# Performance work log

Measured on AMD Instinct MI355X. Metric: run time of the kernel, lower is better.

The kernel has to match this reference:

```python
import jax, jax.numpy as jnp
import numpy as np

LAMBDA = 0.5
ALPHA_PRE = 1.0
ALPHA_DA = 1.0

B, N, C, T, O = 8, 1024, 64, 12, 64


def setup_inputs() -> dict:
    key = jax.random.key(0)
    ks = jax.random.split(key, 10)
    s = 0.1  # keep tanh out of deep saturation, like xavier-init scales
    return {
        "x": jax.random.normal(ks[0], (B, N, C, T), dtype=jnp.float32),
        "static_adj": jax.random.uniform(ks[1], (N, N), dtype=jnp.float32) / N,
        "W0": jax.random.normal(ks[2], (C, O), dtype=jnp.float32) * s,
        "b0": jax.random.normal(ks[3], (O,), dtype=jnp.float32) * s,
        "Ws": jax.random.normal(ks[4], (T, C, O), dtype=jnp.float32) * s,
        "bs": jax.random.normal(ks[5], (T, O), dtype=jnp.float32) * s,
        "Wd": jax.random.normal(ks[6], (T, C, O), dtype=jnp.float32) * s,
        "bd": jax.random.normal(ks[7], (T, O), dtype=jnp.float32) * s,
        "E1": jax.random.normal(ks[8], (T, N, O), dtype=jnp.float32) * s,
        "E2": jax.random.normal(ks[9], (T, N, O), dtype=jnp.float32) * s,
    }


def reference(x, static_adj, W0, b0, Ws, bs, Wd, bd, E1, E2):
    # x: [B,N,C,T] -> [T,B,N,C] so the per-timestep layers vectorize over leading T.
    xt = jnp.transpose(x, (3, 0, 1, 2))  # [T,B,N,C]
    n = xt.shape[2]

    # shared top-level linear
    x0 = jnp.einsum('tbnc,co->tbno', xt, W0) + b0  # [T,B,N,O]

    # static GCN per timestep: linear(static_adj @ x_t)
    sagg = jnp.einsum('nm,tbmc->tbnc', static_adj, xt)
    static_out = jnp.einsum('tbnc,tco->tbno', sagg, Ws) + bs[:, None, None, :]

    # dynamic GCN: base = linear_t(x_t)
    base = jnp.einsum('tbnc,tco->tbno', xt, Wd) + bd[:, None, None, :]
    DE1 = jnp.tanh(ALPHA_PRE * (base * E1[:, None]))  # [T,B,N,O]
    DE2 = jnp.tanh(ALPHA_PRE * (base * E2[:, None]))
    # cross = DE1@DE2^T - DE2@DE1^T = M - M^T
    M = jnp.einsum('tbno,tbmo->tbnm', DE1, DE2)  # [T,B,N,N]
    DA = jax.nn.relu(jnp.tanh(ALPHA_DA * (M - jnp.swapaxes(M, -1, -2))))

    # symmetric degree normalization of (DA + I)
    DA = DA + jnp.eye(n, dtype=DA.dtype)
    rowsum = jnp.clip(DA.sum(axis=-1), 1e-12, None)
    d_inv_sqrt = rowsum ** -0.5
    DA = DA * d_inv_sqrt[..., :, None] * d_inv_sqrt[..., None, :]

    dagg = jnp.einsum('tbnm,tbmc->tbnc', DA, xt)
    dyn_out = jnp.einsum('tbnc,tco->tbno', dagg, Wd) + bd[:, None, None, :]

    fused = (LAMBDA - 0.025) * static_out + (1.0 - LAMBDA - 0.025) * dyn_out + 0.05 * x0
    return jnp.transpose(fused, (1, 2, 3, 0))  # [B,N,O,T]
```

## Files before the change

### kernel.cpp

```cpp
#include <hip/hip_runtime.h>

#define BB 8
#define NN 1024
#define CC 64
#define TT 12
#define OO 64

typedef unsigned short u16;
typedef __attribute__((ext_vector_type(8))) short s16x8;
typedef __attribute__((ext_vector_type(4))) float f32x4;
typedef __attribute__((ext_vector_type(4))) unsigned int u32x4;

__device__ __forceinline__ u16 f2bu(float f){
  union { float f; unsigned u; } v; v.f = f;
  unsigned r = v.u + 0x7FFFu + ((v.u >> 16) & 1u);
  return (u16)(r >> 16);
}
__device__ __forceinline__ float b2f(u16 h){
  union { unsigned u; float f; } v; v.u = ((unsigned)h) << 16; return v.f;
}
__device__ __forceinline__ float relu_tanh(float d){
  float e = __expf(2.0f * d);
  return fmaxf(1.0f - 2.0f * __builtin_amdgcn_rcpf(e + 1.0f), 0.0f);
}
__device__ __forceinline__ float tanh_sgn(float x){
  float ax = fabsf(x);
  float e = __expf(2.0f * ax);
  float t = 1.0f - 2.0f * __builtin_amdgcn_rcpf(e + 1.0f);
  return x < 0.0f ? -t : t;
}

#define MFMA16(a,b,c) __builtin_amdgcn_mfma_f32_16x16x32_bf16((a),(b),(c),0,0,0)

__device__ __forceinline__ s16x8 ld72(const u16* s, int row0, int ko, int lane){
  return *(const s16x8*)(s + (row0 + (lane & 15)) * 72 + ko + ((lane >> 4) << 3));
}

__global__ __launch_bounds__(256) void k0_transpose(const float* __restrict__ x,
                                                    u16* __restrict__ xt){
  const int n = blockIdx.x, b = blockIdx.y;
  __shared__ float s[CC*TT];
  const float* src = x + (size_t)(b*NN + n)*CC*TT;
  for (int k = threadIdx.x; k < CC*TT; k += 256) s[k] = src[k];
  __syncthreads();
  for (int k = threadIdx.x; k < CC*TT; k += 256){
    const int t = k >> 6, c = k & 63;
    xt[(((size_t)t*BB + b)*NN + n)*CC + c] = f2bu(s[c*TT + t]);
  }
}

__global__ __launch_bounds__(256) void kadj(const float* __restrict__ adj,
                                            u16* __restrict__ adjb){
  const size_t i = ((size_t)blockIdx.x*256 + threadIdx.x)*4;
  const float4 v = *(const float4*)(adj + i);
  u16 o0=f2bu(v.x), o1=f2bu(v.y), o2=f2bu(v.z), o3=f2bu(v.w);
  adjb[i]=o0; adjb[i+1]=o1; adjb[i+2]=o2; adjb[i+3]=o3;
}

__global__ __launch_bounds__(256) void k1_de(const u16* __restrict__ xt,
    const float* __restrict__ Wd, const float* __restrict__ bd,
    const float* __restrict__ E1, const float* __restrict__ E2,
    u16* __restrict__ DE1g, u16* __restrict__ DE2g){
  __shared__ __align__(16) u16 sWd[64*72];
  const int tid = threadIdx.x, lane = tid & 63, wid = tid >> 6;
  const int l15 = lane & 15, lr4 = lane >> 4;
  const int it = blockIdx.x, b = blockIdx.y, t = blockIdx.z;
  const int n0 = it * 64;
  for (int k = tid; k < 4096; k += 256){
    const int o = k & 63, c = k >> 6;
    sWd[o*72 + c] = f2bu(Wd[(size_t)t*4096 + c*64 + o]);
  }
  __syncthreads();
  const size_t tb = (size_t)t*BB + b;
  const u16* gx = xt + (tb*NN + n0)*CC;
  const int wrow = wid * 16;
  const f32x4 fz = {0.f,0.f,0.f,0.f};
  f32x4 acc[4] = {fz, fz, fz, fz};
  #pragma unroll
  for (int ks = 0; ks < 2; ++ks){
    const int ko = ks*32;
    const s16x8 a = *(const s16x8*)(gx + (wrow + l15)*CC + ko + (lr4 << 3));
    #pragma unroll
    for (int v = 0; v < 4; ++v)
      acc[v] = MFMA16(a, ld72(sWd, v*16, ko, lane), acc[v]);
  }
  #pragma unroll
  for (int v = 0; v < 4; ++v){
    const int o = v*16 + l15;
    const float bdv = bd[t*OO + o];
    #pragma unroll
    for (int e = 0; e < 4; ++e){
      const int n = n0 + wrow + (lr4 << 2) + e;
      const float base = acc[v][e] + bdv;
      const size_t eo = ((size_t)t*NN + n)*OO + o;
      const size_t so = (tb*NN + n)*OO + o;
      DE1g[so] = f2bu(tanh_sgn(base * E1[eo]));
      DE2g[so] = f2bu(tanh_sgn(base * E2[eo]));
    }
  }
}

__global__ __launch_bounds__(256) void k2a(const u16* __restrict__ DE1g,
    const u16* __restrict__ DE2g, float* __restrict__ dinv){
  __shared__ __align__(16) u16 sB1[64*72], sB2[64*72];
  const int tid = threadIdx.x, lane = tid & 63, wid = tid >> 6;
  const int l15 = lane & 15, lr4 = lane >> 4;
  const int nwg = 16*BB*TT;
  const int logical = ((int)blockIdx.x & 7)*(nwg >> 3) + ((int)blockIdx.x >> 3);
  const int ti = logical & 15;
  const size_t tb = (size_t)(logical >> 4);
  const u16* g1 = DE1g + tb*NN*OO;
  const u16* g2 = DE2g + tb*NN*OO;
  const int i0 = ti * 64;
  for (int k = tid; k < 512; k += 256){
    const int r = k >> 3, c = (k & 7) << 3;
    *(s16x8*)(sB1 + r*72 + c) = *(const s16x8*)(g1 + (size_t)(i0 + r)*OO + c);
    s16x8 v = *(const s16x8*)(g2 + (size_t)(i0 + r)*OO + c);
    u32x4 w = *(u32x4*)&v; w ^= 0x80008000u;
    *(u32x4*)(sB2 + r*72 + c) = w;
  }
  __syncthreads();
  const int wrow = wid * 16;
  s16x8 a1[2], na2[2];
  #pragma unroll
  for (int ks = 0; ks < 2; ++ks){
    a1[ks]  = ld72(sB1, wrow, ks*32, lane);
    na2[ks] = ld72(sB2, wrow, ks*32, lane);
  }
  const int srow = tid >> 2, sc0 = (tid & 3) << 4;
  s16x8 pB1a,pB1b, pB2a,pB2b;
#define LOADT(TJ) do { \
    pB1a = *(const s16x8*)(g2 + (size_t)((TJ)*64 + srow)*OO + sc0); \
    pB1b = *(const s16x8*)(g2 + (size_t)((TJ)*64 + srow)*OO + sc0 + 8); \
    pB2a = *(const s16x8*)(g1 + (size_t)((TJ)*64 + srow)*OO + sc0); \
    pB2b = *(const s16x8*)(g1 + (size_t)((TJ)*64 + srow)*OO + sc0 + 8); \
  } while (0)
  LOADT(0);
  float rp[4] = {0.f,0.f,0.f,0.f};
  const f32x4 fz = {0.f,0.f,0.f,0.f};
  __syncthreads();
  for (int tj = 0; tj < 16; ++tj){
    *(s16x8*)(sB1 + srow*72 + sc0)     = pB1a;
    *(s16x8*)(sB1 + srow*72 + sc0 + 8) = pB1b;
    *(s16x8*)(sB2 + srow*72 + sc0)     = pB2a;
    *(s16x8*)(sB2 + srow*72 + sc0 + 8) = pB2b;
    __syncthreads();
    if (tj < 15) LOADT(tj + 1);
    f32x4 z[4];
    #pragma unroll
    for (int v = 0; v < 4; ++v){
      z[v] = MFMA16(a1[0],  ld72(sB1, v*16, 0,  lane), fz);
      z[v] = MFMA16(na2[0], ld72(sB2, v*16, 0,  lane), z[v]);
      z[v] = MFMA16(a1[1],  ld72(sB1, v*16, 32, lane), z[v]);
      z[v] = MFMA16(na2[1], ld72(sB2, v*16, 32, lane), z[v]);
    }
    #pragma unroll
    for (int v = 0; v < 4; ++v)
      #pragma unroll
      for (int e = 0; e < 4; ++e)
        rp[e] += relu_tanh(z[v][e]);
    __syncthreads();
  }
#undef LOADT
  #pragma unroll
  for (int e = 0; e < 4; ++e){
    float r = rp[e];
    r += __shfl_xor(r, 1); r += __shfl_xor(r, 2);
    r += __shfl_xor(r, 4); r += __shfl_xor(r, 8);
    if (l15 == 0)
      dinv[tb*NN + i0 + wrow + (lr4 << 2) + e] = rsqrtf(r + 1.0f);
  }
}

__global__ __launch_bounds__(256) void k3b(const u16* __restrict__ xt,
    const float* __restrict__ Wd, const float* __restrict__ Ws,
    const float* __restrict__ W0, const float* __restrict__ bd,
    const float* __restrict__ bs, const float* __restrict__ b0,
    const float* __restrict__ dinv, u16* __restrict__ xdvT,
    u16* __restrict__ xswT, u16* __restrict__ x0w){
  __shared__ __align__(16) u16 sW[64*72];
  const int tid = threadIdx.x, lane = tid & 63, wid = tid >> 6;
  const int l15 = lane & 15, lr4 = lane >> 4;
  const int it = blockIdx.x, b = blockIdx.y, t = blockIdx.z;
  const size_t tb = (size_t)t*BB + b;
  const int n0 = it * 128, wrow = wid * 32;
  const float* dvb = dinv + tb*NN + n0;
  float dis[2][4];
  #pragma unroll
  for (int u = 0; u < 2; ++u)
    #pragma unroll
    for (int e = 0; e < 4; ++e)
      dis[u][e] = dvb[wrow + u*16 + (lr4 << 2) + e];
  float badd[4];
  #pragma unroll
  for (int v = 0; v < 4; ++v){
    const int o = v*16 + l15;
    badd[v] = 0.475f*(bd[t*OO + o] + bs[t*OO + o]) + 0.05f*b0[o];
  }
  const u16* gx = xt + (tb*NN + n0)*CC;
  const f32x4 fz = {0.f,0.f,0.f,0.f};
  for (int pass = 0; pass < 3; ++pass){
    __syncthreads();
    {
      const float* Wsrc = (pass == 0) ? (Wd + (size_t)t*4096)
                        : (pass == 1) ? (Ws + (size_t)t*4096) : W0;
      const float scale = (pass == 2) ? 0.05f : 0.475f;
      for (int k = tid; k < 4096; k += 256){
        const int o = k & 63, c = k >> 6;
        sW[o*72 + c] = f2bu(scale * Wsrc[c*64 + o]);
      }
    }
    __syncthreads();
    f32x4 acc[2][4];
    #pragma unroll
    for (int u = 0; u < 2; ++u)
      #pragma unroll
      for (int v = 0; v < 4; ++v) acc[u][v] = fz;
    #pragma unroll
    for (int ks = 0; ks < 2; ++ks){
      const int ko = ks*32;
      s16x8 bw[4];
      #pragma unroll
      for (int v = 0; v < 4; ++v) bw[v] = ld72(sW, v*16, ko, lane);
      #pragma unroll
      for (int u = 0; u < 2; ++u){
        const s16x8 a = *(const s16x8*)(gx + (wrow + u*16 + l15)*CC + ko + (lr4 << 3));
        #pragma unroll
        for (int v = 0; v < 4; ++v) acc[u][v] = MFMA16(a, bw[v], acc[u][v]);
      }
    }
    #pragma unroll
    for (int u = 0; u < 2; ++u)
      #pragma unroll
      for (int v = 0; v < 4; ++v){
        const int o = v*16 + l15;
        #pragma unroll
        for (int e = 0; e < 4; ++e){
          const int nl = wrow + u*16 + (lr4 << 2) + e;
          float val = acc[u][v][e];
          if (pass == 0)      xdvT[(tb*OO + o)*NN + n0 + nl] = f2bu(val * dis[u][e]);
          else if (pass == 1) xswT[(tb*OO + o)*NN + n0 + nl] = f2bu(val);
          else                x0w[(tb*NN + n0 + nl)*OO + o]  = f2bu(val + badd[v]);
        }
      }
  }
}

__global__ __launch_bounds__(256) void k4s(const u16* __restrict__ adjb,
    const u16* __restrict__ xswT, u16* __restrict__ outSta){
  __shared__ __align__(16) u16 sJ[64*72], sS[64*72];
  const int tid = threadIdx.x, lane = tid & 63, wid = tid >> 6;
  const int l15 = lane & 15, lr4 = lane >> 4;
  const int nwg = 16*BB*TT;
  const int logical = ((int)blockIdx.x & 7)*(nwg >> 3) + ((int)blockIdx.x >> 3);
  const int ti = logical / (BB*TT);
  const size_t tb = (size_t)(logical % (BB*TT));
  const u16* xs = xswT + tb*OO*NN;
  const int i0 = ti * 64, wrow = wid * 16;
  const int srow = tid >> 2, sc0 = (tid & 3) << 4;
  s16x8 pJa, pJb, pSa, pSb;
#define LOADS(TJ) do { \
    pJa = *(const s16x8*)(adjb + (size_t)(i0 + srow)*NN + (TJ)*64 + sc0); \
    pJb = *(const s16x8*)(adjb + (size_t)(i0 + srow)*NN + (TJ)*64 + sc0 + 8); \
    pSa = *(const s16x8*)(xs   + (size_t)srow*NN + (TJ)*64 + sc0); \
    pSb = *(const s16x8*)(xs   + (size_t)srow*NN + (TJ)*64 + sc0 + 8); \
  } while (0)
  LOADS(0);
  const f32x4 fz = {0.f,0.f,0.f,0.f};
  f32x4 as_[4] = {fz,fz,fz,fz};
  for (int tj = 0; tj < 16; ++tj){
    *(s16x8*)(sJ + srow*72 + sc0)     = pJa;
    *(s16x8*)(sJ + srow*72 + sc0 + 8) = pJb;
    *(s16x8*)(sS + srow*72 + sc0)     = pSa;
    *(s16x8*)(sS + srow*72 + sc0 + 8) = pSb;
    __syncthreads();
    if (tj < 15) LOADS(tj + 1);
    const s16x8 aJ0 = ld72(sJ, wrow, 0,  lane);
    const s16x8 aJ1 = ld72(sJ, wrow, 32, lane);
    #pragma unroll
    for (int v = 0; v < 4; ++v){
      as_[v] = MFMA16(aJ0, ld72(sS, v*16, 0,  lane), as_[v]);
      as_[v] = MFMA16(aJ1, ld72(sS, v*16, 32, lane), as_[v]);
    }
    __syncthreads();
  }
#undef LOADS
  #pragma unroll
  for (int v = 0; v < 4; ++v){
    const int o = v*16 + l15;
    #pragma unroll
    for (int e = 0; e < 4; ++e){
      const int n = i0 + wrow + (lr4 << 2) + e;
      outSta[(tb*NN + n)*OO + o] = f2bu(as_[v][e]);
    }
  }
}

__global__ __launch_bounds__(256) void k2bf(const u16* __restrict__ DE1g,
    const u16* __restrict__ DE2g, const u16* __restrict__ xdvT,
    const float* __restrict__ dinv, float* __restrict__ outT){
  __shared__ __align__(16) u16 sB1[64*72], sB2[64*72], sXD[64*72];
  __shared__ __align__(16) u16 bounce[4][16*72];
  const int tid = threadIdx.x, lane = tid & 63, wid = tid >> 6;
  const int l15 = lane & 15, lr4 = lane >> 4;
  const int nwg = 16*BB*TT;
  const int logical = ((int)blockIdx.x & 7)*(nwg >> 3) + ((int)blockIdx.x >> 3);
  const int ti = logical & 15;
  const size_t tb = (size_t)(logical >> 4);
  const u16* g1 = DE1g + tb*NN*OO;
  const u16* g2 = DE2g + tb*NN*OO;
  const u16* xd = xdvT + tb*OO*NN;
  const float* dv = dinv + tb*NN;
  const int i0 = ti * 64;
  for (int k = tid; k < 512; k += 256){
    const int r = k >> 3, c = (k & 7) << 3;
    *(s16x8*)(sB1 + r*72 + c) = *(const s16x8*)(g1 + (size_t)(i0 + r)*OO + c);
    s16x8 v = *(const s16x8*)(g2 + (size_t)(i0 + r)*OO + c);
    u32x4 w = *(u32x4*)&v; w ^= 0x80008000u;
    *(u32x4*)(sB2 + r*72 + c) = w;
  }
  __syncthreads();
  const int wrow = wid * 16;
  s16x8 a1[2], na2[2];
  #pragma unroll
  for (int ks = 0; ks < 2; ++ks){
    a1[ks]  = ld72(sB1, wrow, ks*32, lane);
    na2[ks] = ld72(sB2, wrow, ks*32, lane);
  }
  const int srow = tid >> 2, sc0 = (tid & 3) << 4;
  s16x8 pB1a,pB1b, pB2a,pB2b, pXDa,pXDb;
#define LOADT(TJ) do { \
    pB1a = *(const s16x8*)(g2 + (size_t)((TJ)*64 + srow)*OO + sc0); \
    pB1b = *(const s16x8*)(g2 + (size_t)((TJ)*64 + srow)*OO + sc0 + 8); \
    pB2a = *(const s16x8*)(g1 + (size_t)((TJ)*64 + srow)*OO + sc0); \
    pB2b = *(const s16x8*)(g1 + (size_t)((TJ)*64 + srow)*OO + sc0 + 8); \
    pXDa = *(const s16x8*)(xd + (size_t)srow*NN + (TJ)*64 + sc0); \
    pXDb = *(const s16x8*)(xd + (size_t)srow*NN + (TJ)*64 + sc0 + 8); \
  } while (0)
  LOADT(0);
  u16* wb = bounce[wid];
  const f32x4 fz = {0.f,0.f,0.f,0.f};
  f32x4 ad[4] = {fz,fz,fz,fz};
  __syncthreads();
  for (int tj = 0; tj < 16; ++tj){
    *(s16x8*)(sB1 + srow*72 + sc0)     = pB1a;
    *(s16x8*)(sB1 + srow*72 + sc0 + 8) = pB1b;
    *(s16x8*)(sB2 + srow*72 + sc0)     = pB2a;
    *(s16x8*)(sB2 + srow*72 + sc0 + 8) = pB2b;
    *(s16x8*)(sXD + srow*72 + sc0)     = pXDa;
    *(s16x8*)(sXD + srow*72 + sc0 + 8) = pXDb;
    __syncthreads();
    if (tj < 15) LOADT(tj + 1);
    f32x4 z[4];
    #pragma unroll
    for (int v = 0; v < 4; ++v){
      z[v] = MFMA16(a1[0],  ld72(sB1, v*16, 0,  lane), fz);
      z[v] = MFMA16(na2[0], ld72(sB2, v*16, 0,  lane), z[v]);
      z[v] = MFMA16(a1[1],  ld72(sB1, v*16, 32, lane), z[v]);
      z[v] = MFMA16(na2[1], ld72(sB2, v*16, 32, lane), z[v]);
    }
    #pragma unroll
    for (int v = 0; v < 4; ++v)
      #pragma unroll
      for (int e = 0; e < 4; ++e)
        wb[((lr4 << 2) + e)*72 + v*16 + l15] = f2bu(relu_tanh(z[v][e]));
    asm volatile("s_waitcnt lgkmcnt(0)" ::: "memory");
    __builtin_amdgcn_sched_barrier(0);
    s16x8 pa0 = ld72(wb, 0, 0,  lane);
    s16x8 pa1 = ld72(wb, 0, 32, lane);
    #pragma unroll
    for (int v = 0; v < 4; ++v){
      ad[v] = MFMA16(pa0, ld72(sXD, v*16, 0,  lane), ad[v]);
      ad[v] = MFMA16(pa1, ld72(sXD, v*16, 32, lane), ad[v]);
    }
    __syncthreads();
  }
#undef LOADT
  const int grow0 = i0 + wrow + (lr4 << 2);
  float disv[4];
  #pragma unroll
  for (int e = 0; e < 4; ++e) disv[e] = dv[grow0 + e];
  #pragma unroll
  for (int v = 0; v < 4; ++v){
    const int o = v*16 + l15;
    #pragma unroll
    for (int e = 0; e < 4; ++e){
      const float xw = b2f(xd[(size_t)o*NN + grow0 + e]);
      outT[(tb*NN + grow0 + e)*OO + o] = disv[e]*(ad[v][e] + xw);
    }
  }
}

__global__ __launch_bounds__(256) void k5(const float* __restrict__ outT,
                                          const u16* __restrict__ x0w,
                                          const u16* __restrict__ outSta,
                                          float* __restrict__ out){
  __shared__ float s[16*64*12];
  const int tid = threadIdx.x;
  const int nb = blockIdx.x, b = blockIdx.y;
  const int n0 = nb * 16;
  for (int t = 0; t < TT; ++t){
    for (int k = tid; k < 1024; k += 256){
      const int r = k >> 6, o = k & 63;
      const size_t idx = (((size_t)t*BB + b)*NN + n0 + r)*OO + o;
      s[(r*64 + o)*12 + t] = outT[idx] + b2f(x0w[idx]) + b2f(outSta[idx]);
    }
  }
  __syncthreads();
  float* dst = out + (size_t)(b*NN + n0)*OO*TT;
  for (int k = tid; k < 16*64*12; k += 256) dst[k] = s[k];
}

extern "C" void kernel_launch(void* const* d_in, const int* in_sizes, int n_in,
                              void* d_out, int out_size, void* d_ws, size_t ws_size,
                              hipStream_t stream) {
  const float* x   = (const float*)d_in[0];
  const float* adj = (const float*)d_in[1];
  const float* W0  = (const float*)d_in[2];
  const float* b0  = (const float*)d_in[3];
  const float* Ws  = (const float*)d_in[4];
  const float* bs  = (const float*)d_in[5];
  const float* Wd  = (const float*)d_in[6];
  const float* bd  = (const float*)d_in[7];
  const float* E1  = (const float*)d_in[8];
  const float* E2  = (const float*)d_in[9];
  float* out = (float*)d_out;

  char* w = (char*)d_ws;
  size_t off = 0;
  auto take = [&](size_t bytes) -> char* {
    char* p = w + off;
    off += bytes; off = (off + 255) & ~(size_t)255;
    return p;
  };
  const size_t NE = (size_t)TT*BB*NN*OO;
  u16*   xt    = (u16*)  take(NE*2);
  u16*   adjb  = (u16*)  take((size_t)NN*NN*2);
  u16*   DE1   = (u16*)  take(NE*2);
  u16*   DE2   = (u16*)  take(NE*2);
  float* dinv  = (float*)take((size_t)TT*BB*NN*4);
  u16*   xdvT  = (u16*)  take(NE*2);
  u16*   xswT  = (u16*)  take(NE*2);
  u16*   x0w   = (u16*)  take(NE*2);
  u16*   outSta= (u16*)  take(NE*2);
  float* outT  = (float*)take(NE*4);

  k0_transpose<<<dim3(NN, BB), 256, 0, stream>>>(x, xt);
  kadj<<<dim3((NN*NN)/1024), 256, 0, stream>>>(adj, adjb);
  k1_de<<<dim3(16, BB, TT), 256, 0, stream>>>(xt, Wd, bd, E1, E2, DE1, DE2);
  k2a<<<dim3(16*BB*TT), 256, 0, stream>>>(DE1, DE2, dinv);
  k3b<<<dim3(8, BB, TT), 256, 0, stream>>>(xt, Wd, Ws, W0, bd, bs, b0,
                                           dinv, xdvT, xswT, x0w);
  k4s<<<dim3(16*BB*TT), 256, 0, stream>>>(adjb, xswT, outSta);
  k2bf<<<dim3(16*BB*TT), 256, 0, stream>>>(DE1, DE2, xdvT, dinv, outT);
  k5<<<dim3(NN/16, BB), 256, 0, stream>>>(outT, x0w, outSta, out);
}
```

Baseline: 234.1 us.

## Exploit antisymmetry of cross matrix to halve degree computation in k2a

```diff
diff --git a/kernel.cpp b/kernel.cpp
--- a/kernel.cpp
+++ b/kernel.cpp
@@ -22,6 +22,10 @@
 __device__ __forceinline__ float relu_tanh(float d){
   float e = __expf(2.0f * d);
   return fmaxf(1.0f - 2.0f * __builtin_amdgcn_rcpf(e + 1.0f), 0.0f);
+}
+__device__ __forceinline__ float tanh_fast(float d){
+  float e = __expf(2.0f * d);
+  return 1.0f - 2.0f * __builtin_amdgcn_rcpf(e + 1.0f);
 }
 __device__ __forceinline__ float tanh_sgn(float x){
   float ax = fabsf(x);
@@ -55,6 +59,11 @@
   const float4 v = *(const float4*)(adj + i);
   u16 o0=f2bu(v.x), o1=f2bu(v.y), o2=f2bu(v.z), o3=f2bu(v.w);
   adjb[i]=o0; adjb[i+1]=o1; adjb[i+2]=o2; adjb[i+3]=o3;
+}
+
+__global__ __launch_bounds__(256) void kinit(float* __restrict__ rs){
+  const size_t i = (size_t)blockIdx.x*256 + threadIdx.x;
+  if (i < (size_t)TT*BB*NN) rs[i] = 1.0f;
 }
 
 __global__ __launch_bounds__(256) void k1_de(const u16* __restrict__ xt,
@@ -101,32 +110,41 @@
 }
 
 __global__ __launch_bounds__(256) void k2a(const u16* __restrict__ DE1g,
-    const u16* __restrict__ DE2g, float* __restrict__ dinv){
-  __shared__ __align__(16) u16 sB1[64*72], sB2[64*72];
+    const u16* __restrict__ DE2g, float* __restrict__ rowsum){
+  __shared__ __align__(16) u16 s1A[64*72], s2nA[64*72];
+  __shared__ __align__(16) u16 s1B[64*72], s2nB[64*72];
   const int tid = threadIdx.x, lane = tid & 63, wid = tid >> 6;
   const int l15 = lane & 15, lr4 = lane >> 4;
-  const int nwg = 16*BB*TT;
+  const int nwg = 8*BB*TT;
   const int logical = ((int)blockIdx.x & 7)*(nwg >> 3) + ((int)blockIdx.x >> 3);
-  const int ti = logical & 15;
-  const size_t tb = (size_t)(logical >> 4);
+  const int p = logical & 7;
+  const size_t tb = (size_t)(logical >> 3);
+  const int tiA = p, tiB = 15 - p;
   const u16* g1 = DE1g + tb*NN*OO;
   const u16* g2 = DE2g + tb*NN*OO;
-  const int i0 = ti * 64;
   for (int k = tid; k < 512; k += 256){
     const int r = k >> 3, c = (k & 7) << 3;
-    *(s16x8*)(sB1 + r*72 + c) = *(const s16x8*)(g1 + (size_t)(i0 + r)*OO + c);
-    s16x8 v = *(const s16x8*)(g2 + (size_t)(i0 + r)*OO + c);
-    u32x4 w = *(u32x4*)&v; w ^= 0x80008000u;
-    *(u32x4*)(sB2 + r*72 + c) = w;
+    *(s16x8*)(s1A + r*72 + c) = *(const s16x8*)(g1 + (size_t)(tiA*64 + r)*OO + c);
+    s16x8 vA = *(const s16x8*)(g2 + (size_t)(tiA*64 + r)*OO + c);
+    u32x4 wA = *(u32x4*)&vA; wA ^= 0x80008000u;
+    *(u32x4*)(s2nA + r*72 + c) = wA;
+    *(s16x8*)(s1B + r*72 + c) = *(const s16x8*)(g1 + (size_t)(tiB*64 + r)*OO + c);
+    s16x8 vB = *(const s16x8*)(g2 + (size_t)(tiB*64 + r)*OO + c);
+    u32x4 wB = *(u32x4*)&vB; wB ^= 0x80008000u;
+    *(u32x4*)(s2nB + r*72 + c) = wB;
   }
   __syncthreads();
   const int wrow = wid * 16;
-  s16x8 a1[2], na2[2];
+  s16x8 a1A[2], na2A[2], a1B[2], na2B[2];
   #pragma unroll
   for (int ks = 0; ks < 2; ++ks){
-    a1[ks]  = ld72(sB1, wrow, ks*32, lane);
-    na2[ks] = ld72(sB2, wrow, ks*32, lane);
-  }
+    a1A[ks]  = ld72(s1A,  wrow, ks*32, lane);
+    na2A[ks] = ld72(s2nA, wrow, ks*32, lane);
+    a1B[ks]  = ld72(s1B,  wrow, ks*32, lane);
+    na2B[ks] = ld72(s2nB, wrow, ks*32, lane);
+  }
+  u16* sJ1 = s1A;
+  u16* sJ2 = s2nA;
   const int srow = tid >> 2, sc0 = (tid & 3) << 4;
   s16x8 pB1a,pB1b, pB2a,pB2b;
 #define LOADT(TJ) do { \
@@ -135,40 +153,96 @@
     pB2a = *(const s16x8*)(g1 + (size_t)((TJ)*64 + srow)*OO + sc0); \
     pB2b = *(const s16x8*)(g1 + (size_t)((TJ)*64 + srow)*OO + sc0 + 8); \
   } while (0)
-  LOADT(0);
-  float rp[4] = {0.f,0.f,0.f,0.f};
+  LOADT(p);
+  float rpA[4] = {0.f,0.f,0.f,0.f}, rpB[4] = {0.f,0.f,0.f,0.f};
   const f32x4 fz = {0.f,0.f,0.f,0.f};
-  __syncthreads();
-  for (int tj = 0; tj < 16; ++tj){
-    *(s16x8*)(sB1 + srow*72 + sc0)     = pB1a;
-    *(s16x8*)(sB1 + srow*72 + sc0 + 8) = pB1b;
-    *(s16x8*)(sB2 + srow*72 + sc0)     = pB2a;
-    *(s16x8*)(sB2 + srow*72 + sc0 + 8) = pB2b;
+  float* rsg = rowsum + tb*NN;
+  __syncthreads();
+  for (int tj = p; tj < 16; ++tj){
+    *(s16x8*)(sJ1 + srow*72 + sc0)     = pB1a;
+    *(s16x8*)(sJ1 + srow*72 + sc0 + 8) = pB1b;
+    *(s16x8*)(sJ2 + srow*72 + sc0)     = pB2a;
+    *(s16x8*)(sJ2 + srow*72 + sc0 + 8) = pB2b;
     __syncthreads();
     if (tj < 15) LOADT(tj + 1);
-    f32x4 z[4];
+    s16x8 b1[4], b2[4], b1h[4], b2h[4];
     #pragma unroll
     for (int v = 0; v < 4; ++v){
-      z[v] = MFMA16(a1[0],  ld72(sB1, v*16, 0,  lane), fz);
-      z[v] = MFMA16(na2[0], ld72(sB2, v*16, 0,  lane), z[v]);
-      z[v] = MFMA16(a1[1],  ld72(sB1, v*16, 32, lane), z[v]);
-      z[v] = MFMA16(na2[1], ld72(sB2, v*16, 32, lane), z[v]);
-    }
-    #pragma unroll
-    for (int v = 0; v < 4; ++v)
-      #pragma unroll
-      for (int e = 0; e < 4; ++e)
-        rp[e] += relu_tanh(z[v][e]);
+      b1[v]  = ld72(sJ1, v*16, 0,  lane);
+      b2[v]  = ld72(sJ2, v*16, 0,  lane);
+      b1h[v] = ld72(sJ1, v*16, 32, lane);
+      b2h[v] = ld72(sJ2, v*16, 32, lane);
+    }
+    {
+      f32x4 z[4];
+      #pragma unroll
+      for (int v = 0; v < 4; ++v){
+        z[v] = MFMA16(a1A[0],  b1[v],  fz);
+        z[v] = MFMA16(na2A[0], b2[v],  z[v]);
+        z[v] = MFMA16(a1A[1],  b1h[v], z[v]);
+        z[v] = MFMA16(na2A[1], b2h[v], z[v]);
+      }
+      float colp[4] = {0.f,0.f,0.f,0.f};
+      #pragma unroll
+      for (int v = 0; v < 4; ++v)
+        #pragma unroll
+        for (int e = 0; e < 4; ++e){
+          const float th = tanh_fast(z[v][e]);
+          rpA[e]  += fmaxf(th, 0.f);
+          colp[v] += fmaxf(-th, 0.f);
+        }
+      if (tj > tiA){
+        #pragma unroll
+        for (int v = 0; v < 4; ++v){
+          float c = colp[v];
+          c += __shfl_xor(c, 16); c += __shfl_xor(c, 32);
+          if (lane < 16) atomicAdd(&rsg[tj*64 + v*16 + lane], c);
+        }
+      }
+    }
+    if (tj >= tiB){
+      f32x4 z[4];
+      #pragma unroll
+      for (int v = 0; v < 4; ++v){
+        z[v] = MFMA16(a1B[0],  b1[v],  fz);
+        z[v] = MFMA16(na2B[0], b2[v],  z[v]);
+        z[v] = MFMA16(a1B[1],  b1h[v], z[v]);
+        z[v] = MFMA16(na2B[1], b2h[v], z[v]);
+      }
+      float colp[4] = {0.f,0.f,0.f,0.f};
+      #pragma unroll
+      for (int v = 0; v < 4; ++v)
+        #pragma unroll
+        for (int e = 0; e < 4; ++e){
+          const float th = tanh_fast(z[v][e]);
+          rpB[e]  += fmaxf(th, 0.f);
+          colp[v] += fmaxf(-th, 0.f);
+        }
+      if (tj > tiB){
+        #pragma unroll
+        for (int v = 0; v < 4; ++v){
+          float c = colp[v];
+          c += __shfl_xor(c, 16); c += __shfl_xor(c, 32);
+          if (lane < 16) atomicAdd(&rsg[tj*64 + v*16 + lane], c);
+        }
+      }
+    }
     __syncthreads();
   }
 #undef LOADT
   #pragma unroll
   for (int e = 0; e < 4; ++e){
-    float r = rp[e];
+    float r = rpA[e];
     r += __shfl_xor(r, 1); r += __shfl_xor(r, 2);
     r += __shfl_xor(r, 4); r += __shfl_xor(r, 8);
-    if (l15 == 0)
-      dinv[tb*NN + i0 + wrow + (lr4 << 2) + e] = rsqrtf(r + 1.0f);
+    if (l15 == 0) atomicAdd(&rsg[tiA*64 + wrow + (lr4 << 2) + e], r);
+  }
+  #pragma unroll
+  for (int e = 0; e < 4; ++e){
+    float r = rpB[e];
+    r += __shfl_xor(r, 1); r += __shfl_xor(r, 2);
+    r += __shfl_xor(r, 4); r += __shfl_xor(r, 8);
+    if (l15 == 0) atomicAdd(&rsg[tiB*64 + wrow + (lr4 << 2) + e], r);
   }
 }
 
@@ -176,7 +250,7 @@
     const float* __restrict__ Wd, const float* __restrict__ Ws,
     const float* __restrict__ W0, const float* __restrict__ bd,
     const float* __restrict__ bs, const float* __restrict__ b0,
-    const float* __restrict__ dinv, u16* __restrict__ xdvT,
+    const float* __restrict__ rowsum, u16* __restrict__ xdvT,
     u16* __restrict__ xswT, u16* __restrict__ x0w){
   __shared__ __align__(16) u16 sW[64*72];
   const int tid = threadIdx.x, lane = tid & 63, wid = tid >> 6;
@@ -184,13 +258,13 @@
   const int it = blockIdx.x, b = blockIdx.y, t = blockIdx.z;
   const size_t tb = (size_t)t*BB + b;
   const int n0 = it * 128, wrow = wid * 32;
-  const float* dvb = dinv + tb*NN + n0;
+  const float* dvb = rowsum + tb*NN + n0;
   float dis[2][4];
   #pragma unroll
   for (int u = 0; u < 2; ++u)
     #pragma unroll
     for (int e = 0; e < 4; ++e)
-      dis[u][e] = dvb[wrow + u*16 + (lr4 << 2) + e];
+      dis[u][e] = rsqrtf(dvb[wrow + u*16 + (lr4 << 2) + e]);
   float badd[4];
   #pragma unroll
   for (int v = 0; v < 4; ++v){
@@ -298,7 +372,7 @@
 
 __global__ __launch_bounds__(256) void k2bf(const u16* __restrict__ DE1g,
     const u16* __restrict__ DE2g, const u16* __restrict__ xdvT,
-    const float* __restrict__ dinv, float* __restrict__ outT){
+    const float* __restrict__ rowsum, float* __restrict__ outT){
   __shared__ __align__(16) u16 sB1[64*72], sB2[64*72], sXD[64*72];
   __shared__ __align__(16) u16 bounce[4][16*72];
   const int tid = threadIdx.x, lane = tid & 63, wid = tid >> 6;
@@ -310,7 +384,7 @@
   const u16* g1 = DE1g + tb*NN*OO;
   const u16* g2 = DE2g + tb*NN*OO;
   const u16* xd = xdvT + tb*OO*NN;
-  const float* dv = dinv + tb*NN;
+  const float* dv = rowsum + tb*NN;
   const int i0 = ti * 64;
   for (int k = tid; k < 512; k += 256){
     const int r = k >> 3, c = (k & 7) << 3;
@@ -379,7 +453,7 @@
   const int grow0 = i0 + wrow + (lr4 << 2);
   float disv[4];
   #pragma unroll
-  for (int e = 0; e < 4; ++e) disv[e] = dv[grow0 + e];
+  for (int e = 0; e < 4; ++e) disv[e] = rsqrtf(dv[grow0 + e]);
   #pragma unroll
   for (int v = 0; v < 4; ++v){
     const int o = v*16 + l15;
@@ -438,7 +512,7 @@
   u16*   adjb  = (u16*)  take((size_t)NN*NN*2);
   u16*   DE1   = (u16*)  take(NE*2);
   u16*   DE2   = (u16*)  take(NE*2);
-  float* dinv  = (float*)take((size_t)TT*BB*NN*4);
+  float* rowsum= (float*)take((size_t)TT*BB*NN*4);
   u16*   xdvT  = (u16*)  take(NE*2);
   u16*   xswT  = (u16*)  take(NE*2);
   u16*   x0w   = (u16*)  take(NE*2);
@@ -447,11 +521,12 @@
 
   k0_transpose<<<dim3(NN, BB), 256, 0, stream>>>(x, xt);
   kadj<<<dim3((NN*NN)/1024), 256, 0, stream>>>(adj, adjb);
+  kinit<<<dim3((TT*BB*NN + 255)/256), 256, 0, stream>>>(rowsum);
   k1_de<<<dim3(16, BB, TT), 256, 0, stream>>>(xt, Wd, bd, E1, E2, DE1, DE2);
-  k2a<<<dim3(16*BB*TT), 256, 0, stream>>>(DE1, DE2, dinv);
+  k2a<<<dim3(8*BB*TT), 256, 0, stream>>>(DE1, DE2, rowsum);
   k3b<<<dim3(8, BB, TT), 256, 0, stream>>>(xt, Wd, Ws, W0, bd, bs, b0,
-                                           dinv, xdvT, xswT, x0w);
+                                           rowsum, xdvT, xswT, x0w);
   k4s<<<dim3(16*BB*TT), 256, 0, stream>>>(adjb, xswT, outSta);
-  k2bf<<<dim3(16*BB*TT), 256, 0, stream>>>(DE1, DE2, xdvT, dinv, outT);
+  k2bf<<<dim3(16*BB*TT), 256, 0, stream>>>(DE1, DE2, xdvT, rowsum, outT);
   k5<<<dim3(NN/16, BB), 256, 0, stream>>>(outT, x0w, outSta, out);
 }
```

After: 227.8 us. -2.7%, faster.
